# Kernel tuning notes

Measured on AMD Instinct MI355X. Metric: run time of the kernel, lower is better.

## Reference

```python
import jax, jax.numpy as jnp
import numpy as np

N = 4096        # num_queries == gnn_query_dim
C1 = 1001       # classes + 1
D = 4096        # gnn_query_dim
H_MLP = 1024    # mlp_hidden_dim
H = 256         # hidden_dim
O = 256         # output_dim
TOP_K = 32
BN_EPS = 1e-5


def setup_inputs() -> dict:
    key = jax.random.key(0)
    ks = jax.random.split(key, 14)
    def lin(kw, fan_in, shape):
        s = 1.0 / np.sqrt(fan_in)
        return jax.random.uniform(kw, shape, jnp.float32, -s, s)
    return {
        "probs": jax.random.uniform(ks[0], (N, C1), jnp.float32),
        "bbox_coords": jax.random.uniform(ks[1], (N, 4), jnp.float32),
        "query_emb": jax.random.normal(ks[2], (N, D), jnp.float32) * 0.02,
        "node_emb": jax.random.normal(ks[3], (N, D), jnp.float32) * 0.02,
        "mlp_w1": lin(ks[4], D + 4 + C1, (D + 4 + C1, H_MLP)),
        "mlp_b1": lin(ks[5], D + 4 + C1, (H_MLP,)),
        "mlp_w2": lin(ks[6], H_MLP, (H_MLP, N)),
        "mlp_b2": lin(ks[7], H_MLP, (N,)),
        "conv_w1": lin(ks[8], D, (D, H)),
        "conv_b1": lin(ks[9], D, (H,)),
        "conv_w2": lin(ks[10], H, (H, O)),
        "conv_b2": lin(ks[11], H, (O,)),
        "bn_gamma": jnp.ones((H,), jnp.float32),
        "bn_beta": jnp.zeros((H,), jnp.float32),
    }


def reference(probs, bbox_coords, query_emb, node_emb,
              mlp_w1, mlp_b1, mlp_w2, mlp_b2,
              conv_w1, conv_b1, conv_w2, conv_b2,
              bn_gamma, bn_beta):
    # edge-weight MLP -> dense dynamic adjacency logits (N, N)
    ew_in = jnp.concatenate([query_emb, probs, bbox_coords], axis=-1)
    h = jax.nn.relu(ew_in @ mlp_w1 + mlp_b1)
    adj = h @ mlp_w2 + mlp_b2                      # (N, N)

    # top-k neighbors per node (sparse dynamic graph)
    vals, idx = jax.lax.top_k(adj, TOP_K)          # (N, K), (N, K)

    # GCN symmetric normalization from row-degree (sum of top-k weights)
    deg = jnp.sum(vals, axis=-1)                   # (N,)
    dinv = jnp.where(deg > 0, jax.lax.rsqrt(jnp.maximum(deg, 1e-12)), 0.0)
    wn = vals * dinv[:, None] * dinv[idx]          # (N, K)

    def gcn_conv(x, w, b):
        # gather neighbor features, weighted sum, then linear
        msg = jnp.einsum('nk,nkf->nf', wn, x[idx])  # (N, F)
        return msg @ w + b

    out = gcn_conv(node_emb, conv_w1, conv_b1)      # (N, H)
    # BatchNorm1d (batch statistics, training-mode math)
    mean = jnp.mean(out, axis=0)
    var = jnp.var(out, axis=0)
    out = (out - mean) * jax.lax.rsqrt(var + BN_EPS) * bn_gamma + bn_beta
    out = jax.nn.relu(out)
    # dropout is identity in eval mode
    out = gcn_conv(out, conv_w2, conv_b2)           # (N, O)
    return out
```

## Files before the change

kernel.cpp:

```cpp
#include <hip/hip_runtime.h>
#include <cfloat>

#define N_NODES 4096
#define C1_DIM  1001
#define D_DIM   4096
#define HMLP    1024
#define KCAT    (D_DIM + C1_DIM + 4)
#define K1PAD   5120
#define TOPK    32

typedef unsigned short u16;
typedef __bf16 bf16x8 __attribute__((ext_vector_type(8)));
typedef float  f32x4  __attribute__((ext_vector_type(4)));

__device__ __forceinline__ unsigned rne_bits(float x) {
  const unsigned u = __float_as_uint(x);
  return u + 0x7FFFu + ((u >> 16) & 1u);
}

__device__ __forceinline__ void gload16(const void* g, void* l) {
  __builtin_amdgcn_global_load_lds(
      (const __attribute__((address_space(1))) unsigned int*)g,
      (__attribute__((address_space(3))) unsigned int*)l, 16, 0, 0);
}

__device__ __forceinline__ void transpose_body(
    const float* __restrict__ in, int R, int C, int Rpad,
    u16* __restrict__ out_hi, u16* __restrict__ out_lo,
    int bxi, int byi, float (*t)[65]) {
  const int rb = bxi * 64;
  const int cb = byi * 64;
  const int tid = threadIdx.x;
  const int lr = tid >> 6, lc = tid & 63;
#pragma unroll
  for (int i = 0; i < 16; ++i) {
    const int r = lr + i * 4;
    const int gr = rb + r;
    t[r][lc] = (gr < R) ? in[(size_t)gr * C + cb + lc] : 0.f;
  }
  __syncthreads();
#pragma unroll
  for (int i = 0; i < 16; ++i) {
    const int c = lr + i * 4;
    const float v = t[lc][c];
    const unsigned vh = rne_bits(v);
    const float r = v - __uint_as_float(vh & 0xFFFF0000u);
    const size_t o = (size_t)(cb + c) * Rpad + rb + lc;
    out_hi[o] = (u16)(vh >> 16);
    out_lo[o] = (u16)(rne_bits(r) >> 16);
  }
}

__device__ __forceinline__ void a_split_body(
    const float* __restrict__ query, const float* __restrict__ probs,
    const float* __restrict__ bbox,
    u16* __restrict__ hi, u16* __restrict__ lo, int blk) {
  const size_t idx = ((size_t)blk * 256 + threadIdx.x) * 8;
  const int row = (int)(idx / K1PAD);
  const int col = (int)(idx - (size_t)row * K1PAD);
  float xs[8];
  if (col < D_DIM) {
    const float4 x0 = *(const float4*)(query + (size_t)row * D_DIM + col);
    const float4 x1 = *(const float4*)(query + (size_t)row * D_DIM + col + 4);
    xs[0]=x0.x; xs[1]=x0.y; xs[2]=x0.z; xs[3]=x0.w;
    xs[4]=x1.x; xs[5]=x1.y; xs[6]=x1.z; xs[7]=x1.w;
  } else {
#pragma unroll
    for (int e = 0; e < 8; ++e) {
      const int c = col + e - D_DIM;
      xs[e] = (c < C1_DIM) ? probs[(size_t)row * C1_DIM + c]
            : (c < C1_DIM + 4) ? bbox[(size_t)row * 4 + (c - C1_DIM)] : 0.f;
    }
  }
  unsigned hw[4], lw[4];
#pragma unroll
  for (int p = 0; p < 4; ++p) {
    const unsigned v0 = rne_bits(xs[2*p]);
    const unsigned v1 = rne_bits(xs[2*p+1]);
    hw[p] = (v1 & 0xFFFF0000u) | (v0 >> 16);
    const float r0 = xs[2*p]   - __uint_as_float(v0 & 0xFFFF0000u);
    const float r1 = xs[2*p+1] - __uint_as_float(v1 & 0xFFFF0000u);
    lw[p] = (rne_bits(r1) & 0xFFFF0000u) | (rne_bits(r0) >> 16);
  }
  *(uint4*)(hi + idx) = make_uint4(hw[0], hw[1], hw[2], hw[3]);
  *(uint4*)(lo + idx) = make_uint4(lw[0], lw[1], lw[2], lw[3]);
}

__global__ __launch_bounds__(256) void prep1_kernel(
    const float* __restrict__ query, const float* __restrict__ probs,
    const float* __restrict__ bbox, const float* __restrict__ mlp_w1,
    u16* __restrict__ a_hi, u16* __restrict__ a_lo,
    u16* __restrict__ w1t_hi, u16* __restrict__ w1t_lo) {
  __shared__ float t[64][65];
  const int b = blockIdx.x;
  if (b < 10240) {
    a_split_body(query, probs, bbox, a_hi, a_lo, b);
  } else {
    const int bb = b - 10240;
    transpose_body(mlp_w1, KCAT, HMLP, K1PAD, w1t_hi, w1t_lo,
                   bb % 80, bb / 80, t);
  }
}

__global__ __launch_bounds__(256) void prep2_kernel(
    const float* __restrict__ mlp_w2, const float* __restrict__ conv_w1,
    u16* __restrict__ w2t_hi, u16* __restrict__ w2t_lo,
    u16* __restrict__ w1ct_hi, u16* __restrict__ w1ct_lo) {
  __shared__ float t[64][65];
  const int b = blockIdx.x;
  if (b < 1024) {
    transpose_body(mlp_w2, HMLP, N_NODES, HMLP, w2t_hi, w2t_lo,
                   b & 15, b >> 4, t);
  } else {
    const int bb = b - 1024;
    transpose_body(conv_w1, D_DIM, 256, D_DIM, w1ct_hi, w1ct_lo,
                   bb & 63, bb >> 6, t);
  }
}


template<bool RELU, bool OUT_SPLIT, bool HASBIAS>
__device__ __forceinline__ void epilogue_64(
    f32x4 (&acc)[4][2], int row0, int col0, int wr0, int wc0, int lane,
    const float* bias, float* Cf, u16* Chi, u16* Clo, int N) {
#pragma unroll
  for (int mi = 0; mi < 4; ++mi)
#pragma unroll
    for (int ni = 0; ni < 2; ++ni) {
      const int gcol = col0 + wc0 + ni * 16 + (lane & 15);
      const float b = HASBIAS ? bias[gcol] : 0.f;
#pragma unroll
      for (int r = 0; r < 4; ++r) {
        const int grow = row0 + wr0 + mi * 16 + (lane >> 4) * 4 + r;
        float v = acc[mi][ni][r] + b;
        if (RELU) v = fmaxf(v, 0.f);
        if (OUT_SPLIT) {
          const unsigned vh = rne_bits(v);
          Chi[(size_t)grow * N + gcol] = (u16)(vh >> 16);
          const float rr = v - __uint_as_float(vh & 0xFFFF0000u);
          Clo[(size_t)grow * N + gcol] = (u16)(rne_bits(rr) >> 16);
        } else {
          Cf[(size_t)grow * N + gcol] = v;
        }
      }
    }
}

template<bool RELU, bool OUT_SPLIT, bool HASBIAS>
__device__ __forceinline__ void gemm_pipe3(
    int bx, int by,
    const u16* __restrict__ Ahi, const u16* __restrict__ Alo, int lda,
    const u16* __restrict__ Bthi, const u16* __restrict__ Btlo, int ldb,
    const float* __restrict__ bias,
    float* __restrict__ Cf, u16* __restrict__ Chi, u16* __restrict__ Clo,
    int N, int K, u16* lds) {
  const int tid = threadIdx.x;
  const int lane = tid & 63, wave = tid >> 6;
  const int row0 = by * 128, col0 = bx * 64;
  const int wr0 = (wave >> 1) * 64, wc0 = (wave & 1) * 32;
  const int srow = tid >> 2;
  const int sk   = ((tid & 3) ^ ((tid >> 3) & 3)) * 8;
  const int wu   = (tid & ~63) * 8;

  f32x4 acc[4][2];
#pragma unroll
  for (int mi = 0; mi < 4; ++mi)
#pragma unroll
    for (int ni = 0; ni < 2; ++ni) acc[mi][ni] = (f32x4){0.f, 0.f, 0.f, 0.f};

  auto stage = [&](int buf, int k0) {
    u16* base = lds + buf * 12288;
    gload16(Ahi + (size_t)(row0 + srow) * lda + k0 + sk,      base + wu);
    gload16(Ahi + (size_t)(row0 + 64 + srow) * lda + k0 + sk, base + 2048 + wu);
    gload16(Alo + (size_t)(row0 + srow) * lda + k0 + sk,      base + 4096 + wu);
    gload16(Alo + (size_t)(row0 + 64 + srow) * lda + k0 + sk, base + 6144 + wu);
    gload16(Bthi + (size_t)(col0 + srow) * ldb + k0 + sk, base + 8192 + wu);
    gload16(Btlo + (size_t)(col0 + srow) * ldb + k0 + sk, base + 10240 + wu);
  };
  auto compute = [&](int buf) {
    u16* base = lds + buf * 12288;
    const int ko_swz = ((lane >> 4) ^ ((lane >> 1) & 3)) * 8;
    const int ar = lane & 15;
    bf16x8 ah[4], al[4], bh[2], bl[2];
#pragma unroll
    for (int mi = 0; mi < 4; ++mi) {
      const int r = wr0 + mi * 16 + ar;
      ah[mi] = *(const bf16x8*)&base[r * 32 + ko_swz];
      al[mi] = *(const bf16x8*)&base[4096 + r * 32 + ko_swz];
    }
#pragma unroll
    for (int ni = 0; ni < 2; ++ni) {
      const int c = wc0 + ni * 16 + ar;
      bh[ni] = *(const bf16x8*)&base[8192 + c * 32 + ko_swz];
      bl[ni] = *(const bf16x8*)&base[10240 + c * 32 + ko_swz];
    }
#pragma unroll
    for (int mi = 0; mi < 4; ++mi)
#pragma unroll
      for (int ni = 0; ni < 2; ++ni) {
        acc[mi][ni] = __builtin_amdgcn_mfma_f32_16x16x32_bf16(ah[mi], bh[ni], acc[mi][ni], 0, 0, 0);
        acc[mi][ni] = __builtin_amdgcn_mfma_f32_16x16x32_bf16(ah[mi], bl[ni], acc[mi][ni], 0, 0, 0);
        acc[mi][ni] = __builtin_amdgcn_mfma_f32_16x16x32_bf16(al[mi], bh[ni], acc[mi][ni], 0, 0, 0);
      }
  };

  const int nk = K >> 5;
  stage(0, 0);
  stage(1, 32);
  int cb = 0;
  for (int k = 0; k < nk; ++k) {
    if (k + 2 < nk) {
      int sb = cb + 2; if (sb >= 3) sb -= 3;
      stage(sb, (k + 2) * 32);
      asm volatile("s_waitcnt vmcnt(12)" ::: "memory");
    } else if (k + 1 < nk) {
      asm volatile("s_waitcnt vmcnt(6)" ::: "memory");
    } else {
      asm volatile("s_waitcnt vmcnt(0)" ::: "memory");
    }
    __builtin_amdgcn_s_barrier();
    compute(cb);
    __builtin_amdgcn_s_barrier();
    ++cb; if (cb >= 3) cb -= 3;
  }

  epilogue_64<RELU, OUT_SPLIT, HASBIAS>(acc, row0, col0, wr0, wc0, lane,
                                        bias, Cf, Chi, Clo, N);
}

__device__ __forceinline__ void gemm_a1p(
    int bx, int by,
    const float* __restrict__ Aq, int lda,
    const u16* __restrict__ Bthi, const u16* __restrict__ Btlo, int ldb,
    float* __restrict__ Cf, int N, int K, u16* lds) {
  const int tid = threadIdx.x;
  const int lane = tid & 63, wave = tid >> 6;
  const int row0 = by * 128, col0 = bx * 64;
  const int wr0 = (wave >> 1) * 64, wc0 = (wave & 1) * 32;
  const int srow = tid >> 2;
  const int sk   = ((tid & 3) ^ ((tid >> 3) & 3)) * 8;
  const int wu   = (tid & ~63) * 8;
  const int arowA = tid >> 3;
  const int skA   = ((tid & 7) ^ ((tid >> 3) & 7)) * 4;

  f32x4 acc[4][2];
#pragma unroll
  for (int mi = 0; mi < 4; ++mi)
#pragma unroll
    for (int ni = 0; ni < 2; ++ni) acc[mi][ni] = (f32x4){0.f, 0.f, 0.f, 0.f};

  auto stage = [&](int buf, int k0) {
    u16* base = lds + buf * 12288;
#pragma unroll
    for (int j = 0; j < 4; ++j) {
      gload16(Aq + (size_t)(row0 + 32 * j + arowA) * lda + k0 + skA,
              base + j * 2048 + wu);
    }
    gload16(Bthi + (size_t)(col0 + srow) * ldb + k0 + sk, base + 8192 + wu);
    gload16(Btlo + (size_t)(col0 + srow) * ldb + k0 + sk, base + 10240 + wu);
  };
  auto compute = [&](int buf) {
    u16* base = lds + buf * 12288;
    const float* Af = (const float*)base;
    const int ko_swz = ((lane >> 4) ^ ((lane >> 1) & 3)) * 8;
    const int c = lane >> 4;
    const int ar = lane & 15;
    bf16x8 ah[4], al[4], bh[2], bl[2];
#pragma unroll
    for (int mi = 0; mi < 4; ++mi) {
      const int r = wr0 + mi * 16 + ar;
      const int s = ar & 7;
      const f32x4 a0 = *(const f32x4*)&Af[r * 32 + (((2 * c) ^ s) * 4)];
      const f32x4 a1 = *(const f32x4*)&Af[r * 32 + (((2 * c + 1) ^ s) * 4)];
      const float xs[8] = {a0[0], a0[1], a0[2], a0[3], a1[0], a1[1], a1[2], a1[3]};
      union { u16 u[8]; bf16x8 v; } H, L;
#pragma unroll
      for (int e = 0; e < 8; ++e) {
        const unsigned vh = rne_bits(xs[e]);
        H.u[e] = (u16)(vh >> 16);
        const float rr = xs[e] - __uint_as_float(vh & 0xFFFF0000u);
        L.u[e] = (u16)(rne_bits(rr) >> 16);
      }
      ah[mi] = H.v; al[mi] = L.v;
    }
#pragma unroll
    for (int ni = 0; ni < 2; ++ni) {
      const int cc = wc0 + ni * 16 + ar;
      bh[ni] = *(const bf16x8*)&base[8192 + cc * 32 + ko_swz];
      bl[ni] = *(const bf16x8*)&base[10240 + cc * 32 + ko_swz];
    }
#pragma unroll
    for (int mi = 0; mi < 4; ++mi)
#pragma unroll
      for (int ni = 0; ni < 2; ++ni) {
        acc[mi][ni] = __builtin_amdgcn_mfma_f32_16x16x32_bf16(ah[mi], bh[ni], acc[mi][ni], 0, 0, 0);
        acc[mi][ni] = __builtin_amdgcn_mfma_f32_16x16x32_bf16(ah[mi], bl[ni], acc[mi][ni], 0, 0, 0);
        acc[mi][ni] = __builtin_amdgcn_mfma_f32_16x16x32_bf16(al[mi], bh[ni], acc[mi][ni], 0, 0, 0);
      }
  };

  const int nk = K >> 5;
  stage(0, 0);
  stage(1, 32);
  int cb = 0;
  for (int k = 0; k < nk; ++k) {
    if (k + 2 < nk) {
      int sb = cb + 2; if (sb >= 3) sb -= 3;
      stage(sb, (k + 2) * 32);
      asm volatile("s_waitcnt vmcnt(12)" ::: "memory");
    } else if (k + 1 < nk) {
      asm volatile("s_waitcnt vmcnt(6)" ::: "memory");
    } else {
      asm volatile("s_waitcnt vmcnt(0)" ::: "memory");
    }
    __builtin_amdgcn_s_barrier();
    compute(cb);
    __builtin_amdgcn_s_barrier();
    ++cb; if (cb >= 3) cb -= 3;
  }

  epilogue_64<false, false, false>(acc, row0, col0, wr0, wc0, lane,
                                   nullptr, Cf, nullptr, nullptr, N);
}

template<bool HASBIAS>
__device__ __forceinline__ void gemm_pipe128(
    int bx, int by,
    const u16* __restrict__ Ahi, const u16* __restrict__ Alo, int lda,
    const u16* __restrict__ Bthi, const u16* __restrict__ Btlo, int ldb,
    const float* __restrict__ bias, float* __restrict__ Cf,
    int N, int K, u16* lds) {
  const int tid = threadIdx.x;
  const int lane = tid & 63, wave = tid >> 6;
  const int row0 = by * 128, col0 = bx * 128;
  const int wr0 = (wave >> 1) * 64, wc0 = (wave & 1) * 64;
  const int srow = tid >> 2;
  const int sk   = ((tid & 3) ^ ((tid >> 3) & 3)) * 8;
  const int wu   = (tid & ~63) * 8;

  f32x4 acc[4][4];
#pragma unroll
  for (int mi = 0; mi < 4; ++mi)
#pragma unroll
    for (int ni = 0; ni < 4; ++ni) acc[mi][ni] = (f32x4){0.f, 0.f, 0.f, 0.f};

  auto stage = [&](int buf, int k0) {
    u16* base = lds + buf * 16384;
    gload16(Ahi + (size_t)(row0 + srow) * lda + k0 + sk,      base + wu);
    gload16(Ahi + (size_t)(row0 + 64 + srow) * lda + k0 + sk, base + 2048 + wu);
    gload16(Alo + (size_t)(row0 + srow) * lda + k0 + sk,      base + 4096 + wu);
    gload16(Alo + (size_t)(row0 + 64 + srow) * lda + k0 + sk, base + 6144 + wu);
    gload16(Bthi + (size_t)(col0 + srow) * ldb + k0 + sk,      base + 8192 + wu);
    gload16(Bthi + (size_t)(col0 + 64 + srow) * ldb + k0 + sk, base + 10240 + wu);
    gload16(Btlo + (size_t)(col0 + srow) * ldb + k0 + sk,      base + 12288 + wu);
    gload16(Btlo + (size_t)(col0 + 64 + srow) * ldb + k0 + sk, base + 14336 + wu);
  };
  auto compute = [&](int buf) {
    u16* base = lds + buf * 16384;
    const int ko_swz = ((lane >> 4) ^ ((lane >> 1) & 3)) * 8;
    const int ar = lane & 15;
    bf16x8 ah[4], al[4], bh[4], bl[4];
#pragma unroll
    for (int mi = 0; mi < 4; ++mi) {
      const int r = wr0 + mi * 16 + ar;
      ah[mi] = *(const bf16x8*)&base[r * 32 + ko_swz];
      al[mi] = *(const bf16x8*)&base[4096 + r * 32 + ko_swz];
    }
#pragma unroll
    for (int ni = 0; ni < 4; ++ni) {
      const int c = wc0 + ni * 16 + ar;
      bh[ni] = *(const bf16x8*)&base[8192 + c * 32 + ko_swz];
      bl[ni] = *(const bf16x8*)&base[12288 + c * 32 + ko_swz];
    }
#pragma unroll
    for (int mi = 0; mi < 4; ++mi)
#pragma unroll
      for (int ni = 0; ni < 4; ++ni) {
        acc[mi][ni] = __builtin_amdgcn_mfma_f32_16x16x32_bf16(ah[mi], bh[ni], acc[mi][ni], 0, 0, 0);
        acc[mi][ni] = __builtin_amdgcn_mfma_f32_16x16x32_bf16(ah[mi], bl[ni], acc[mi][ni], 0, 0, 0);
        acc[mi][ni] = __builtin_amdgcn_mfma_f32_16x16x32_bf16(al[mi], bh[ni], acc[mi][ni], 0, 0, 0);
      }
  };

  const int nk = K >> 5;
  stage(0, 0);
  int cur = 0;
  for (int k = 0; k < nk; ++k) {
    if (k + 1 < nk) {
      stage(cur ^ 1, (k + 1) * 32);
      asm volatile("s_waitcnt vmcnt(8)" ::: "memory");
    } else {
      asm volatile("s_waitcnt vmcnt(0)" ::: "memory");
    }
    __builtin_amdgcn_s_barrier();
    compute(cur);
    __builtin_amdgcn_s_barrier();
    cur ^= 1;
  }

#pragma unroll
  for (int mi = 0; mi < 4; ++mi)
#pragma unroll
    for (int ni = 0; ni < 4; ++ni) {
      const int gcol = col0 + wc0 + ni * 16 + (lane & 15);
      const float b = HASBIAS ? bias[gcol] : 0.f;
#pragma unroll
      for (int r = 0; r < 4; ++r) {
        const int grow = row0 + wr0 + mi * 16 + (lane >> 4) * 4 + r;
        Cf[(size_t)grow * N + gcol] = acc[mi][ni][r] + b;
      }
    }
}

__global__ __launch_bounds__(256, 2) void gemm1_kernel(
    const u16* __restrict__ a_hi, const u16* __restrict__ a_lo,
    const u16* __restrict__ w1t_hi, const u16* __restrict__ w1t_lo,
    const float* __restrict__ b1,
    u16* __restrict__ h_hi, u16* __restrict__ h_lo) {
  __shared__ u16 lds[3 * 12288];
  const int r = blockIdx.x;
  const int x = r & 7;
  const int i = r >> 3;
  const int by = x * 4 + (i >> 4);
  const int bx = i & 15;
  gemm_pipe3<true, true, true>(bx, by,
      a_hi, a_lo, K1PAD, w1t_hi, w1t_lo, K1PAD, b1,
      nullptr, h_hi, h_lo, HMLP, K1PAD, lds);
}

__global__ __launch_bounds__(256, 2) void fused2_kernel(
    const u16* __restrict__ h_hi, const u16* __restrict__ h_lo,
    const u16* __restrict__ w2t_hi, const u16* __restrict__ w2t_lo,
    const float* __restrict__ b2, float* __restrict__ adj,
    const float* __restrict__ node,
    const u16* __restrict__ w1ct_hi, const u16* __restrict__ w1ct_lo,
    float* __restrict__ Z1) {
  __shared__ u16 lds[3 * 12288];
  const int bid = blockIdx.x;
  if (bid < 128) {
    const int x = bid & 7;
    const int i = bid >> 3;
    const int by = x * 4 + (i >> 2);
    const int bx = i & 3;
    gemm_a1p(bx, by,
             node, D_DIM, w1ct_hi, w1ct_lo, D_DIM,
             Z1, 256, D_DIM, lds);
  } else {
    const int r = bid - 128;
    const int x = r & 7;
    const int i = r >> 3;
    const int rg = x >> 1, cg = x & 1;
    const int by = rg * 8 + (i >> 4);
    const int bx = cg * 16 + (i & 15);
    gemm_pipe128<true>(bx, by,
        h_hi, h_lo, HMLP, w2t_hi, w2t_lo, HMLP, b2,
        adj, N_NODES, HMLP, lds);
  }
}

__global__ __launch_bounds__(256) void gemm_small_bn(
    const float* __restrict__ A, const float* __restrict__ colstats,
    const float* __restrict__ gamma, const float* __restrict__ beta,
    const float* __restrict__ B, float* __restrict__ C,
    int M, int Ncols, int K) {
  __shared__ float As[16][68];
  __shared__ float Bs[16][68];
  const int tid = threadIdx.x;
  const int row0 = blockIdx.y * 64, col0 = blockIdx.x * 64;
  const int tx = tid & 15, ty = tid >> 4;
  const int arow = tid >> 2, acol = (tid & 3) * 4;
  const int brow = tid >> 4, bcol = (tid & 15) * 4;

  float acc[4][4];
#pragma unroll
  for (int i = 0; i < 4; ++i)
#pragma unroll
    for (int j = 0; j < 4; ++j) acc[i][j] = 0.f;

  for (int k0 = 0; k0 < K; k0 += 16) {
    float4 a4 = *(const float4*)(A + (size_t)(row0 + arow) * K + k0 + acol);
    float av4[4] = {a4.x, a4.y, a4.z, a4.w};
#pragma unroll
    for (int e = 0; e < 4; ++e) {
      const int c = k0 + acol + e;
      const float mean = colstats[c] * (1.f / 4096.f);
      float var = colstats[256 + c] * (1.f / 4096.f) - mean * mean;
      var = fmaxf(var, 0.f);
      const float v = (av4[e] - mean) * rsqrtf(var + 1e-5f) * gamma[c] + beta[c];
      av4[e] = fmaxf(v, 0.f);
    }
    const float4 b4 = *(const float4*)(B + (size_t)(k0 + brow) * Ncols + col0 + bcol);
    __syncthreads();
    As[acol + 0][arow] = av4[0]; As[acol + 1][arow] = av4[1];
    As[acol + 2][arow] = av4[2]; As[acol + 3][arow] = av4[3];
    *(float4*)&Bs[brow][bcol] = b4;
    __syncthreads();
#pragma unroll
    for (int k = 0; k < 16; ++k) {
      float av[4], bw[4];
      *(float4*)&av[0] = *(const float4*)&As[k][ty * 4];
      *(float4*)&bw[0] = *(const float4*)&Bs[k][tx * 4];
#pragma unroll
      for (int i = 0; i < 4; ++i)
#pragma unroll
        for (int j = 0; j < 4; ++j) acc[i][j] += av[i] * bw[j];
    }
  }

#pragma unroll
  for (int i = 0; i < 4; ++i) {
    const int r = row0 + ty * 4 + i;
    float4 v;
    v.x = acc[i][0]; v.y = acc[i][1]; v.z = acc[i][2]; v.w = acc[i][3];
    *(float4*)(C + (size_t)r * Ncols + col0 + tx * 4) = v;
  }
}

__global__ __launch_bounds__(256) void topk_kernel(
    const float* __restrict__ adj, float* __restrict__ vals,
    int* __restrict__ idxo, float* __restrict__ dinv) {
  __shared__ float sv[N_NODES];
  __shared__ float rw[4];
  __shared__ int   iw[4];
  const int n = blockIdx.x, tid = threadIdx.x;
  const int lane = tid & 63, wave = tid >> 6;
  const float4* rowp = (const float4*)(adj + (size_t)n * N_NODES);

  float mv = -FLT_MAX; int mi = 0x7FFFFFFF;
  for (int g = tid; g < N_NODES / 4; g += 256) {
    const float4 v4 = rowp[g];
    *(float4*)&sv[g * 4] = v4;
    if (v4.x > mv) { mv = v4.x; mi = g * 4 + 0; }
    if (v4.y > mv) { mv = v4.y; mi = g * 4 + 1; }
    if (v4.z > mv) { mv = v4.z; mi = g * 4 + 2; }
    if (v4.w > mv) { mv = v4.w; mi = g * 4 + 3; }
  }

  float sum = 0.f;
  for (int it = 0; it < TOPK; ++it) {
    float bv = mv; int bi = mi;
#pragma unroll
    for (int off = 1; off < 64; off <<= 1) {
      const float ov = __shfl_xor(bv, off);
      const int   oi = __shfl_xor(bi, off);
      if (ov > bv || (ov == bv && oi < bi)) { bv = ov; bi = oi; }
    }
    if (lane == 0) { rw[wave] = bv; iw[wave] = bi; }
    __syncthreads();
    bv = rw[0]; bi = iw[0];
#pragma unroll
    for (int w = 1; w < 4; ++w) {
      const float ov = rw[w]; const int oi = iw[w];
      if (ov > bv || (ov == bv && oi < bi)) { bv = ov; bi = oi; }
    }
    if (tid == 0) {
      vals[(size_t)n * TOPK + it] = bv;
      idxo[(size_t)n * TOPK + it] = bi;
    }
    sum += bv;
    if (tid == ((bi >> 2) & 255)) {
      sv[bi] = -FLT_MAX;
      mv = -FLT_MAX; mi = 0x7FFFFFFF;
      for (int g = tid; g < N_NODES / 4; g += 256) {
#pragma unroll
        for (int e = 0; e < 4; ++e) {
          const float v = sv[g * 4 + e];
          if (v > mv) { mv = v; mi = g * 4 + e; }
        }
      }
    }
    __syncthreads();
  }
  if (tid == 0)
    dinv[n] = (sum > 0.f) ? rsqrtf(fmaxf(sum, 1e-12f)) : 0.f;
}

__global__ __launch_bounds__(256) void agg_kernel(
    const float* __restrict__ Z, const float* __restrict__ vals,
    const int* __restrict__ idxo, const float* __restrict__ dinv,
    const float* __restrict__ bias, float* __restrict__ out) {
  const int n = blockIdx.x, f = threadIdx.x;
  const float dn = dinv[n];
  float acc = bias[f];
#pragma unroll
  for (int k = 0; k < TOPK; ++k) {
    const int   j = idxo[n * TOPK + k];
    const float w = vals[n * TOPK + k] * dn * dinv[j];
    acc += w * Z[(size_t)j * 256 + f];
  }
  out[(size_t)n * 256 + f] = acc;
}

__global__ __launch_bounds__(256) void bn_partial(
    const float* __restrict__ x, float* __restrict__ partial) {
  const int b = blockIdx.x, c = threadIdx.x;
  float s = 0.f, s2 = 0.f;
  for (int r = b * 32; r < b * 32 + 32; ++r) {
    const float v = x[(size_t)r * 256 + c];
    s += v; s2 += v * v;
  }
  partial[(size_t)b * 512 + c]       = s;
  partial[(size_t)b * 512 + 256 + c] = s2;
}

__global__ __launch_bounds__(256) void bn_reduce(
    const float* __restrict__ partial, float* __restrict__ colstats) {
  const int j = blockIdx.x, t = threadIdx.x;
  __shared__ float red[128];
  if (t < 128) red[t] = partial[(size_t)t * 512 + j];
  __syncthreads();
  for (int s = 64; s > 0; s >>= 1) {
    if (t < s) red[t] += red[t + s];
    __syncthreads();
  }
  if (t == 0) colstats[j] = red[0];
}

extern "C" void kernel_launch(void* const* d_in, const int* in_sizes, int n_in,
                              void* d_out, int out_size, void* d_ws, size_t ws_size,
                              hipStream_t stream) {
  const float* probs   = (const float*)d_in[0];
  const float* bbox    = (const float*)d_in[1];
  const float* query   = (const float*)d_in[2];
  const float* node    = (const float*)d_in[3];
  const float* mlp_w1  = (const float*)d_in[4];
  const float* mlp_b1  = (const float*)d_in[5];
  const float* mlp_w2  = (const float*)d_in[6];
  const float* mlp_b2  = (const float*)d_in[7];
  const float* conv_w1 = (const float*)d_in[8];
  const float* conv_b1 = (const float*)d_in[9];
  const float* conv_w2 = (const float*)d_in[10];
  const float* conv_b2 = (const float*)d_in[11];
  const float* gamma   = (const float*)d_in[12];
  const float* beta    = (const float*)d_in[13];

  float* ws = (float*)d_ws;
  size_t off = 0;
  float* R1 = ws + off;  off += (size_t)N_NODES * K1PAD;
  u16* a_hi = (u16*)R1;
  u16* a_lo = a_hi + (size_t)N_NODES * K1PAD;
  float* adj = R1;
  float* spare = R1 + (size_t)N_NODES * N_NODES;
  float* Z1   = spare;
  float* vals = spare + (size_t)N_NODES * 256;
  int*   idxo = (int*)(vals + (size_t)N_NODES * TOPK);
  float* dinv = (float*)idxo + (size_t)N_NODES * TOPK;
  float* partial  = dinv + N_NODES;
  float* colstats = partial + 128 * 512;
  float* R2 = ws + off;  off += (size_t)HMLP * K1PAD;
  u16* w1t_hi = (u16*)R2;
  u16* w1t_lo = w1t_hi + (size_t)HMLP * K1PAD;
  u16* w2t_hi = (u16*)R2;
  u16* w2t_lo = w2t_hi + (size_t)N_NODES * HMLP;
  u16* w1ct_hi = (u16*)(R2 + (size_t)N_NODES * HMLP);
  u16* w1ct_lo = w1ct_hi + (size_t)256 * D_DIM;
  float* out1 = R2 + (size_t)N_NODES * HMLP;
  float* R3 = ws + off;  off += (size_t)N_NODES * HMLP;
  u16* h_hi = (u16*)R3;
  u16* h_lo = h_hi + (size_t)N_NODES * HMLP;
  float* Z2 = adj;

  prep1_kernel<<<10240 + 1280, 256, 0, stream>>>(
      query, probs, bbox, mlp_w1, a_hi, a_lo, w1t_hi, w1t_lo);
  gemm1_kernel<<<512, 256, 0, stream>>>(
      a_hi, a_lo, w1t_hi, w1t_lo, mlp_b1, h_hi, h_lo);
  prep2_kernel<<<1024 + 256, 256, 0, stream>>>(
      mlp_w2, conv_w1, w2t_hi, w2t_lo, w1ct_hi, w1ct_lo);
  fused2_kernel<<<128 + (N_NODES / 128) * (N_NODES / 128), 256, 0, stream>>>(
      h_hi, h_lo, w2t_hi, w2t_lo, mlp_b2, adj, node, w1ct_hi, w1ct_lo, Z1);
  topk_kernel<<<N_NODES, 256, 0, stream>>>(adj, vals, idxo, dinv);
  agg_kernel<<<N_NODES, 256, 0, stream>>>(Z1, vals, idxo, dinv, conv_b1, out1);
  bn_partial<<<128, 256, 0, stream>>>(out1, partial);
  bn_reduce<<<512, 256, 0, stream>>>(partial, colstats);
  gemm_small_bn<<<dim3(256 / 64, N_NODES / 64), 256, 0, stream>>>(
      out1, colstats, gamma, beta, conv_w2, Z2, N_NODES, 256, 256);
  agg_kernel<<<N_NODES, 256, 0, stream>>>(Z2, vals, idxo, dinv, conv_b2, (float*)d_out);
}
```

Measured before the change: 521.6 us.

## Enlarge adjacency GEMM tile to 256x256 with 512-thread blocks

```diff
diff --git a/kernel.cpp b/kernel.cpp
--- a/kernel.cpp
+++ b/kernel.cpp
@@ -229,11 +229,11 @@
 }
 
 __device__ __forceinline__ void gemm_a1p(
-    int bx, int by,
+    int ltid, int bx, int by,
     const float* __restrict__ Aq, int lda,
     const u16* __restrict__ Bthi, const u16* __restrict__ Btlo, int ldb,
     float* __restrict__ Cf, int N, int K, u16* lds) {
-  const int tid = threadIdx.x;
+  const int tid = ltid;
   const int lane = tid & 63, wave = tid >> 6;
   const int row0 = by * 128, col0 = bx * 64;
   const int wr0 = (wave >> 1) * 64, wc0 = (wave & 1) * 32;
@@ -321,95 +321,6 @@
 
   epilogue_64<false, false, false>(acc, row0, col0, wr0, wc0, lane,
                                    nullptr, Cf, nullptr, nullptr, N);
-}
-
-template<bool HASBIAS>
-__device__ __forceinline__ void gemm_pipe128(
-    int bx, int by,
-    const u16* __restrict__ Ahi, const u16* __restrict__ Alo, int lda,
-    const u16* __restrict__ Bthi, const u16* __restrict__ Btlo, int ldb,
-    const float* __restrict__ bias, float* __restrict__ Cf,
-    int N, int K, u16* lds) {
-  const int tid = threadIdx.x;
-  const int lane = tid & 63, wave = tid >> 6;
-  const int row0 = by * 128, col0 = bx * 128;
-  const int wr0 = (wave >> 1) * 64, wc0 = (wave & 1) * 64;
-  const int srow = tid >> 2;
-  const int sk   = ((tid & 3) ^ ((tid >> 3) & 3)) * 8;
-  const int wu   = (tid & ~63) * 8;
-
-  f32x4 acc[4][4];
-#pragma unroll
-  for (int mi = 0; mi < 4; ++mi)
-#pragma unroll
-    for (int ni = 0; ni < 4; ++ni) acc[mi][ni] = (f32x4){0.f, 0.f, 0.f, 0.f};
-
-  auto stage = [&](int buf, int k0) {
-    u16* base = lds + buf * 16384;
-    gload16(Ahi + (size_t)(row0 + srow) * lda + k0 + sk,      base + wu);
-    gload16(Ahi + (size_t)(row0 + 64 + srow) * lda + k0 + sk, base + 2048 + wu);
-    gload16(Alo + (size_t)(row0 + srow) * lda + k0 + sk,      base + 4096 + wu);
-    gload16(Alo + (size_t)(row0 + 64 + srow) * lda + k0 + sk, base + 6144 + wu);
-    gload16(Bthi + (size_t)(col0 + srow) * ldb + k0 + sk,      base + 8192 + wu);
-    gload16(Bthi + (size_t)(col0 + 64 + srow) * ldb + k0 + sk, base + 10240 + wu);
-    gload16(Btlo + (size_t)(col0 + srow) * ldb + k0 + sk,      base + 12288 + wu);
-    gload16(Btlo + (size_t)(col0 + 64 + srow) * ldb + k0 + sk, base + 14336 + wu);
-  };
-  auto compute = [&](int buf) {
-    u16* base = lds + buf * 16384;
-    const int ko_swz = ((lane >> 4) ^ ((lane >> 1) & 3)) * 8;
-    const int ar = lane & 15;
-    bf16x8 ah[4], al[4], bh[4], bl[4];
-#pragma unroll
-    for (int mi = 0; mi < 4; ++mi) {
-      const int r = wr0 + mi * 16 + ar;
-      ah[mi] = *(const bf16x8*)&base[r * 32 + ko_swz];
-      al[mi] = *(const bf16x8*)&base[4096 + r * 32 + ko_swz];
-    }
-#pragma unroll
-    for (int ni = 0; ni < 4; ++ni) {
-      const int c = wc0 + ni * 16 + ar;
-      bh[ni] = *(const bf16x8*)&base[8192 + c * 32 + ko_swz];
-      bl[ni] = *(const bf16x8*)&base[12288 + c * 32 + ko_swz];
-    }
-#pragma unroll
-    for (int mi = 0; mi < 4; ++mi)
-#pragma unroll
-      for (int ni = 0; ni < 4; ++ni) {
-        acc[mi][ni] = __builtin_amdgcn_mfma_f32_16x16x32_bf16(ah[mi], bh[ni], acc[mi][ni], 0, 0, 0);
-        acc[mi][ni] = __builtin_amdgcn_mfma_f32_16x16x32_bf16(ah[mi], bl[ni], acc[mi][ni], 0, 0, 0);
-        acc[mi][ni] = __builtin_amdgcn_mfma_f32_16x16x32_bf16(al[mi], bh[ni], acc[mi][ni], 0, 0, 0);
-      }
-  };
-
-  const int nk = K >> 5;
-  stage(0, 0);
-  int cur = 0;
-  for (int k = 0; k < nk; ++k) {
-    if (k + 1 < nk) {
-      stage(cur ^ 1, (k + 1) * 32);
-      asm volatile("s_waitcnt vmcnt(8)" ::: "memory");
-    } else {
-      asm volatile("s_waitcnt vmcnt(0)" ::: "memory");
-    }
-    __builtin_amdgcn_s_barrier();
-    compute(cur);
-    __builtin_amdgcn_s_barrier();
-    cur ^= 1;
-  }
-
-#pragma unroll
-  for (int mi = 0; mi < 4; ++mi)
-#pragma unroll
-    for (int ni = 0; ni < 4; ++ni) {
-      const int gcol = col0 + wc0 + ni * 16 + (lane & 15);
-      const float b = HASBIAS ? bias[gcol] : 0.f;
-#pragma unroll
-      for (int r = 0; r < 4; ++r) {
-        const int grow = row0 + wr0 + mi * 16 + (lane >> 4) * 4 + r;
-        Cf[(size_t)grow * N + gcol] = acc[mi][ni][r] + b;
-      }
-    }
 }
 
 __global__ __launch_bounds__(256, 2) void gemm1_kernel(
@@ -428,34 +339,112 @@
       nullptr, h_hi, h_lo, HMLP, K1PAD, lds);
 }
 
-__global__ __launch_bounds__(256, 2) void fused2_kernel(
+__global__ __launch_bounds__(512, 1) void adj_kernel(
     const u16* __restrict__ h_hi, const u16* __restrict__ h_lo,
     const u16* __restrict__ w2t_hi, const u16* __restrict__ w2t_lo,
     const float* __restrict__ b2, float* __restrict__ adj,
     const float* __restrict__ node,
     const u16* __restrict__ w1ct_hi, const u16* __restrict__ w1ct_lo,
     float* __restrict__ Z1) {
-  __shared__ u16 lds[3 * 12288];
+  __shared__ u16 lds[73728];
   const int bid = blockIdx.x;
-  if (bid < 128) {
-    const int x = bid & 7;
-    const int i = bid >> 3;
-    const int by = x * 4 + (i >> 2);
-    const int bx = i & 3;
-    gemm_a1p(bx, by,
+  if (bid < 64) {
+    const int half = threadIdx.x >> 8;
+    const int ltid = threadIdx.x & 255;
+    const int by = bid >> 1;
+    const int bx = (bid & 1) * 2 + half;
+    gemm_a1p(ltid, bx, by,
              node, D_DIM, w1ct_hi, w1ct_lo, D_DIM,
-             Z1, 256, D_DIM, lds);
-  } else {
-    const int r = bid - 128;
-    const int x = r & 7;
-    const int i = r >> 3;
-    const int rg = x >> 1, cg = x & 1;
-    const int by = rg * 8 + (i >> 4);
-    const int bx = cg * 16 + (i & 15);
-    gemm_pipe128<true>(bx, by,
-        h_hi, h_lo, HMLP, w2t_hi, w2t_lo, HMLP, b2,
-        adj, N_NODES, HMLP, lds);
-  }
+             Z1, 256, D_DIM, lds + half * 36864);
+    return;
+  }
+  const int r = bid - 64;
+  const int x = r & 7;
+  const int i = r >> 3;
+  const int rg = x >> 1, cg = x & 1;
+  const int by = rg * 4 + (i >> 3);
+  const int bx = cg * 8 + (i & 7);
+
+  const int lda = HMLP, ldb = HMLP, N = N_NODES, K = HMLP;
+  const int tid = threadIdx.x;
+  const int lane = tid & 63, wave = tid >> 6;
+  const int row0 = by * 256, col0 = bx * 256;
+  const int wr0 = (wave >> 2) * 128;
+  const int wc0 = (wave & 3) * 64;
+  const int srow = tid >> 2;
+  const int sk   = ((tid & 3) ^ ((tid >> 3) & 3)) * 8;
+  const int wu   = (tid & ~63) * 8;
+
+  f32x4 acc[8][4];
+#pragma unroll
+  for (int mi = 0; mi < 8; ++mi)
+#pragma unroll
+    for (int ni = 0; ni < 4; ++ni) acc[mi][ni] = (f32x4){0.f, 0.f, 0.f, 0.f};
+
+  auto stage = [&](int buf, int k0) {
+    u16* base = lds + buf * 32768;
+    gload16(h_hi + (size_t)(row0 + srow) * lda + k0 + sk,       base + wu);
+    gload16(h_hi + (size_t)(row0 + 128 + srow) * lda + k0 + sk, base + 4096 + wu);
+    gload16(h_lo + (size_t)(row0 + srow) * lda + k0 + sk,       base + 8192 + wu);
+    gload16(h_lo + (size_t)(row0 + 128 + srow) * lda + k0 + sk, base + 12288 + wu);
+    gload16(w2t_hi + (size_t)(col0 + srow) * ldb + k0 + sk,       base + 16384 + wu);
+    gload16(w2t_hi + (size_t)(col0 + 128 + srow) * ldb + k0 + sk, base + 20480 + wu);
+    gload16(w2t_lo + (size_t)(col0 + srow) * ldb + k0 + sk,       base + 24576 + wu);
+    gload16(w2t_lo + (size_t)(col0 + 128 + srow) * ldb + k0 + sk, base + 28672 + wu);
+  };
+  auto compute = [&](int buf) {
+    u16* base = lds + buf * 32768;
+    const int ko_swz = ((lane >> 4) ^ ((lane >> 1) & 3)) * 8;
+    const int ar = lane & 15;
+    bf16x8 bh[4], bl[4];
+#pragma unroll
+    for (int ni = 0; ni < 4; ++ni) {
+      const int c = wc0 + ni * 16 + ar;
+      bh[ni] = *(const bf16x8*)&base[16384 + c * 32 + ko_swz];
+      bl[ni] = *(const bf16x8*)&base[24576 + c * 32 + ko_swz];
+    }
+#pragma unroll
+    for (int mi = 0; mi < 8; ++mi) {
+      const int rr2 = wr0 + mi * 16 + ar;
+      const bf16x8 ah = *(const bf16x8*)&base[rr2 * 32 + ko_swz];
+      const bf16x8 al = *(const bf16x8*)&base[8192 + rr2 * 32 + ko_swz];
+#pragma unroll
+      for (int ni = 0; ni < 4; ++ni) {
+        acc[mi][ni] = __builtin_amdgcn_mfma_f32_16x16x32_bf16(ah, bh[ni], acc[mi][ni], 0, 0, 0);
+        acc[mi][ni] = __builtin_amdgcn_mfma_f32_16x16x32_bf16(ah, bl[ni], acc[mi][ni], 0, 0, 0);
+        acc[mi][ni] = __builtin_amdgcn_mfma_f32_16x16x32_bf16(al, bh[ni], acc[mi][ni], 0, 0, 0);
+      }
+    }
+  };
+
+  const int nk = K >> 5;
+  stage(0, 0);
+  int cur = 0;
+  for (int k = 0; k < nk; ++k) {
+    if (k + 1 < nk) {
+      stage(cur ^ 1, (k + 1) * 32);
+      asm volatile("s_waitcnt vmcnt(8)" ::: "memory");
+    } else {
+      asm volatile("s_waitcnt vmcnt(0)" ::: "memory");
+    }
+    __builtin_amdgcn_s_barrier();
+    compute(cur);
+    __builtin_amdgcn_s_barrier();
+    cur ^= 1;
+  }
+
+#pragma unroll
+  for (int mi = 0; mi < 8; ++mi)
+#pragma unroll
+    for (int ni = 0; ni < 4; ++ni) {
+      const int gcol = col0 + wc0 + ni * 16 + (lane & 15);
+      const float b = b2[gcol];
+#pragma unroll
+      for (int rr3 = 0; rr3 < 4; ++rr3) {
+        const int grow = row0 + wr0 + mi * 16 + (lane >> 4) * 4 + rr3;
+        adj[(size_t)grow * N + gcol] = acc[mi][ni][rr3] + b;
+      }
+    }
 }
 
 __global__ __launch_bounds__(256) void gemm_small_bn(
@@ -666,7 +655,7 @@
       a_hi, a_lo, w1t_hi, w1t_lo, mlp_b1, h_hi, h_lo);
   prep2_kernel<<<1024 + 256, 256, 0, stream>>>(
       mlp_w2, conv_w1, w2t_hi, w2t_lo, w1ct_hi, w1ct_lo);
-  fused2_kernel<<<128 + (N_NODES / 128) * (N_NODES / 128), 256, 0, stream>>>(
+  adj_kernel<<<320, 512, 0, stream>>>(
       h_hi, h_lo, w2t_hi, w2t_lo, mlp_b2, adj, node, w1ct_hi, w1ct_lo, Z1);
   topk_kernel<<<N_NODES, 256, 0, stream>>>(adj, vals, idxo, dinv);
   agg_kernel<<<N_NODES, 256, 0, stream>>>(Z1, vals, idxo, dinv, conv_b1, out1);
```

Result: slower. 601.9 us (+15.4%).

## Fuse fp32 activation hi/lo split into first MLP GEMM instead of prep pass

Applied to the files above, without the earlier changes.

```diff
diff --git a/kernel.cpp b/kernel.cpp
--- a/kernel.cpp
+++ b/kernel.cpp
@@ -51,52 +51,35 @@
   }
 }
 
-__device__ __forceinline__ void a_split_body(
-    const float* __restrict__ query, const float* __restrict__ probs,
-    const float* __restrict__ bbox,
-    u16* __restrict__ hi, u16* __restrict__ lo, int blk) {
-  const size_t idx = ((size_t)blk * 256 + threadIdx.x) * 8;
-  const int row = (int)(idx / K1PAD);
-  const int col = (int)(idx - (size_t)row * K1PAD);
-  float xs[8];
-  if (col < D_DIM) {
-    const float4 x0 = *(const float4*)(query + (size_t)row * D_DIM + col);
-    const float4 x1 = *(const float4*)(query + (size_t)row * D_DIM + col + 4);
-    xs[0]=x0.x; xs[1]=x0.y; xs[2]=x0.z; xs[3]=x0.w;
-    xs[4]=x1.x; xs[5]=x1.y; xs[6]=x1.z; xs[7]=x1.w;
-  } else {
-#pragma unroll
-    for (int e = 0; e < 8; ++e) {
-      const int c = col + e - D_DIM;
-      xs[e] = (c < C1_DIM) ? probs[(size_t)row * C1_DIM + c]
-            : (c < C1_DIM + 4) ? bbox[(size_t)row * 4 + (c - C1_DIM)] : 0.f;
-    }
-  }
-  unsigned hw[4], lw[4];
-#pragma unroll
-  for (int p = 0; p < 4; ++p) {
-    const unsigned v0 = rne_bits(xs[2*p]);
-    const unsigned v1 = rne_bits(xs[2*p+1]);
-    hw[p] = (v1 & 0xFFFF0000u) | (v0 >> 16);
-    const float r0 = xs[2*p]   - __uint_as_float(v0 & 0xFFFF0000u);
-    const float r1 = xs[2*p+1] - __uint_as_float(v1 & 0xFFFF0000u);
-    lw[p] = (rne_bits(r1) & 0xFFFF0000u) | (rne_bits(r0) >> 16);
-  }
-  *(uint4*)(hi + idx) = make_uint4(hw[0], hw[1], hw[2], hw[3]);
-  *(uint4*)(lo + idx) = make_uint4(lw[0], lw[1], lw[2], lw[3]);
+__device__ __forceinline__ void tailf_body(
+    const float* __restrict__ probs, const float* __restrict__ bbox,
+    float* __restrict__ tailF, int blk) {
+  const int i = blk * 256 + threadIdx.x;
+  const int row = i >> 7;
+  const int col = (i & 127) * 8;
+  float v[8];
+#pragma unroll
+  for (int e = 0; e < 8; ++e) {
+    const int c = col + e;
+    v[e] = (c < C1_DIM) ? probs[(size_t)row * C1_DIM + c]
+         : (c < C1_DIM + 4) ? bbox[(size_t)row * 4 + (c - C1_DIM)] : 0.f;
+  }
+  float* dst = tailF + (size_t)row * 1024 + col;
+  *(float4*)dst       = make_float4(v[0], v[1], v[2], v[3]);
+  *(float4*)(dst + 4) = make_float4(v[4], v[5], v[6], v[7]);
 }
 
 __global__ __launch_bounds__(256) void prep1_kernel(
-    const float* __restrict__ query, const float* __restrict__ probs,
-    const float* __restrict__ bbox, const float* __restrict__ mlp_w1,
-    u16* __restrict__ a_hi, u16* __restrict__ a_lo,
+    const float* __restrict__ probs, const float* __restrict__ bbox,
+    const float* __restrict__ mlp_w1,
+    float* __restrict__ tailF,
     u16* __restrict__ w1t_hi, u16* __restrict__ w1t_lo) {
   __shared__ float t[64][65];
   const int b = blockIdx.x;
-  if (b < 10240) {
-    a_split_body(query, probs, bbox, a_hi, a_lo, b);
+  if (b < 2048) {
+    tailf_body(probs, bbox, tailF, b);
   } else {
-    const int bb = b - 10240;
+    const int bb = b - 2048;
     transpose_body(mlp_w1, KCAT, HMLP, K1PAD, w1t_hi, w1t_lo,
                    bb % 80, bb / 80, t);
   }
@@ -146,10 +129,10 @@
     }
 }
 
-template<bool RELU, bool OUT_SPLIT, bool HASBIAS>
-__device__ __forceinline__ void gemm_pipe3(
+template<bool RELU, bool OUT_SPLIT, bool HASBIAS, bool SPLITSRC>
+__device__ __forceinline__ void gemm_a1p(
     int bx, int by,
-    const u16* __restrict__ Ahi, const u16* __restrict__ Alo, int lda,
+    const float* __restrict__ Aq, int lda, const float* __restrict__ Atail,
     const u16* __restrict__ Bthi, const u16* __restrict__ Btlo, int ldb,
     const float* __restrict__ bias,
     float* __restrict__ Cf, u16* __restrict__ Chi, u16* __restrict__ Clo,
@@ -161,6 +144,8 @@
   const int srow = tid >> 2;
   const int sk   = ((tid & 3) ^ ((tid >> 3) & 3)) * 8;
   const int wu   = (tid & ~63) * 8;
+  const int arowA = tid >> 3;
+  const int skA   = ((tid & 7) ^ ((tid >> 3) & 7)) * 4;
 
   f32x4 acc[4][2];
 #pragma unroll
@@ -170,29 +155,46 @@
 
   auto stage = [&](int buf, int k0) {
     u16* base = lds + buf * 12288;
-    gload16(Ahi + (size_t)(row0 + srow) * lda + k0 + sk,      base + wu);
-    gload16(Ahi + (size_t)(row0 + 64 + srow) * lda + k0 + sk, base + 2048 + wu);
-    gload16(Alo + (size_t)(row0 + srow) * lda + k0 + sk,      base + 4096 + wu);
-    gload16(Alo + (size_t)(row0 + 64 + srow) * lda + k0 + sk, base + 6144 + wu);
+    const float* srcA = Aq;
+    int ldaA = lda, kk = k0;
+    if (SPLITSRC && k0 >= D_DIM) { srcA = Atail; ldaA = 1024; kk = k0 - D_DIM; }
+#pragma unroll
+    for (int j = 0; j < 4; ++j) {
+      gload16(srcA + (size_t)(row0 + 32 * j + arowA) * ldaA + kk + skA,
+              base + j * 2048 + wu);
+    }
     gload16(Bthi + (size_t)(col0 + srow) * ldb + k0 + sk, base + 8192 + wu);
     gload16(Btlo + (size_t)(col0 + srow) * ldb + k0 + sk, base + 10240 + wu);
   };
   auto compute = [&](int buf) {
     u16* base = lds + buf * 12288;
+    const float* Af = (const float*)base;
     const int ko_swz = ((lane >> 4) ^ ((lane >> 1) & 3)) * 8;
+    const int c = lane >> 4;
     const int ar = lane & 15;
     bf16x8 ah[4], al[4], bh[2], bl[2];
 #pragma unroll
     for (int mi = 0; mi < 4; ++mi) {
       const int r = wr0 + mi * 16 + ar;
-      ah[mi] = *(const bf16x8*)&base[r * 32 + ko_swz];
-      al[mi] = *(const bf16x8*)&base[4096 + r * 32 + ko_swz];
+      const int s = ar & 7;
+      const f32x4 a0 = *(const f32x4*)&Af[r * 32 + (((2 * c) ^ s) * 4)];
+      const f32x4 a1 = *(const f32x4*)&Af[r * 32 + (((2 * c + 1) ^ s) * 4)];
+      const float xs[8] = {a0[0], a0[1], a0[2], a0[3], a1[0], a1[1], a1[2], a1[3]};
+      union { u16 u[8]; bf16x8 v; } H, L;
+#pragma unroll
+      for (int e = 0; e < 8; ++e) {
+        const unsigned vh = rne_bits(xs[e]);
+        H.u[e] = (u16)(vh >> 16);
+        const float rr = xs[e] - __uint_as_float(vh & 0xFFFF0000u);
+        L.u[e] = (u16)(rne_bits(rr) >> 16);
+      }
+      ah[mi] = H.v; al[mi] = L.v;
     }
 #pragma unroll
     for (int ni = 0; ni < 2; ++ni) {
-      const int c = wc0 + ni * 16 + ar;
-      bh[ni] = *(const bf16x8*)&base[8192 + c * 32 + ko_swz];
-      bl[ni] = *(const bf16x8*)&base[10240 + c * 32 + ko_swz];
+      const int cc = wc0 + ni * 16 + ar;
+      bh[ni] = *(const bf16x8*)&base[8192 + cc * 32 + ko_swz];
+      bl[ni] = *(const bf16x8*)&base[10240 + cc * 32 + ko_swz];
     }
 #pragma unroll
     for (int mi = 0; mi < 4; ++mi)
@@ -226,101 +228,6 @@
 
   epilogue_64<RELU, OUT_SPLIT, HASBIAS>(acc, row0, col0, wr0, wc0, lane,
                                         bias, Cf, Chi, Clo, N);
-}
-
-__device__ __forceinline__ void gemm_a1p(
-    int bx, int by,
-    const float* __restrict__ Aq, int lda,
-    const u16* __restrict__ Bthi, const u16* __restrict__ Btlo, int ldb,
-    float* __restrict__ Cf, int N, int K, u16* lds) {
-  const int tid = threadIdx.x;
-  const int lane = tid & 63, wave = tid >> 6;
-  const int row0 = by * 128, col0 = bx * 64;
-  const int wr0 = (wave >> 1) * 64, wc0 = (wave & 1) * 32;
-  const int srow = tid >> 2;
-  const int sk   = ((tid & 3) ^ ((tid >> 3) & 3)) * 8;
-  const int wu   = (tid & ~63) * 8;
-  const int arowA = tid >> 3;
-  const int skA   = ((tid & 7) ^ ((tid >> 3) & 7)) * 4;
-
-  f32x4 acc[4][2];
-#pragma unroll
-  for (int mi = 0; mi < 4; ++mi)
-#pragma unroll
-    for (int ni = 0; ni < 2; ++ni) acc[mi][ni] = (f32x4){0.f, 0.f, 0.f, 0.f};
-
-  auto stage = [&](int buf, int k0) {
-    u16* base = lds + buf * 12288;
-#pragma unroll
-    for (int j = 0; j < 4; ++j) {
-      gload16(Aq + (size_t)(row0 + 32 * j + arowA) * lda + k0 + skA,
-              base + j * 2048 + wu);
-    }
-    gload16(Bthi + (size_t)(col0 + srow) * ldb + k0 + sk, base + 8192 + wu);
-    gload16(Btlo + (size_t)(col0 + srow) * ldb + k0 + sk, base + 10240 + wu);
-  };
-  auto compute = [&](int buf) {
-    u16* base = lds + buf * 12288;
-    const float* Af = (const float*)base;
-    const int ko_swz = ((lane >> 4) ^ ((lane >> 1) & 3)) * 8;
-    const int c = lane >> 4;
-    const int ar = lane & 15;
-    bf16x8 ah[4], al[4], bh[2], bl[2];
-#pragma unroll
-    for (int mi = 0; mi < 4; ++mi) {
-      const int r = wr0 + mi * 16 + ar;
-      const int s = ar & 7;
-      const f32x4 a0 = *(const f32x4*)&Af[r * 32 + (((2 * c) ^ s) * 4)];
-      const f32x4 a1 = *(const f32x4*)&Af[r * 32 + (((2 * c + 1) ^ s) * 4)];
-      const float xs[8] = {a0[0], a0[1], a0[2], a0[3], a1[0], a1[1], a1[2], a1[3]};
-      union { u16 u[8]; bf16x8 v; } H, L;
-#pragma unroll
-      for (int e = 0; e < 8; ++e) {
-        const unsigned vh = rne_bits(xs[e]);
-        H.u[e] = (u16)(vh >> 16);
-        const float rr = xs[e] - __uint_as_float(vh & 0xFFFF0000u);
-        L.u[e] = (u16)(rne_bits(rr) >> 16);
-      }
-      ah[mi] = H.v; al[mi] = L.v;
-    }
-#pragma unroll
-    for (int ni = 0; ni < 2; ++ni) {
-      const int cc = wc0 + ni * 16 + ar;
-      bh[ni] = *(const bf16x8*)&base[8192 + cc * 32 + ko_swz];
-      bl[ni] = *(const bf16x8*)&base[10240 + cc * 32 + ko_swz];
-    }
-#pragma unroll
-    for (int mi = 0; mi < 4; ++mi)
-#pragma unroll
-      for (int ni = 0; ni < 2; ++ni) {
-        acc[mi][ni] = __builtin_amdgcn_mfma_f32_16x16x32_bf16(ah[mi], bh[ni], acc[mi][ni], 0, 0, 0);
-        acc[mi][ni] = __builtin_amdgcn_mfma_f32_16x16x32_bf16(ah[mi], bl[ni], acc[mi][ni], 0, 0, 0);
-        acc[mi][ni] = __builtin_amdgcn_mfma_f32_16x16x32_bf16(al[mi], bh[ni], acc[mi][ni], 0, 0, 0);
-      }
-  };
-
-  const int nk = K >> 5;
-  stage(0, 0);
-  stage(1, 32);
-  int cb = 0;
-  for (int k = 0; k < nk; ++k) {
-    if (k + 2 < nk) {
-      int sb = cb + 2; if (sb >= 3) sb -= 3;
-      stage(sb, (k + 2) * 32);
-      asm volatile("s_waitcnt vmcnt(12)" ::: "memory");
-    } else if (k + 1 < nk) {
-      asm volatile("s_waitcnt vmcnt(6)" ::: "memory");
-    } else {
-      asm volatile("s_waitcnt vmcnt(0)" ::: "memory");
-    }
-    __builtin_amdgcn_s_barrier();
-    compute(cb);
-    __builtin_amdgcn_s_barrier();
-    ++cb; if (cb >= 3) cb -= 3;
-  }
-
-  epilogue_64<false, false, false>(acc, row0, col0, wr0, wc0, lane,
-                                   nullptr, Cf, nullptr, nullptr, N);
 }
 
 template<bool HASBIAS>
@@ -413,7 +320,7 @@
 }
 
 __global__ __launch_bounds__(256, 2) void gemm1_kernel(
-    const u16* __restrict__ a_hi, const u16* __restrict__ a_lo,
+    const float* __restrict__ query, const float* __restrict__ tailF,
     const u16* __restrict__ w1t_hi, const u16* __restrict__ w1t_lo,
     const float* __restrict__ b1,
     u16* __restrict__ h_hi, u16* __restrict__ h_lo) {
@@ -423,8 +330,8 @@
   const int i = r >> 3;
   const int by = x * 4 + (i >> 4);
   const int bx = i & 15;
-  gemm_pipe3<true, true, true>(bx, by,
-      a_hi, a_lo, K1PAD, w1t_hi, w1t_lo, K1PAD, b1,
+  gemm_a1p<true, true, true, true>(bx, by,
+      query, D_DIM, tailF, w1t_hi, w1t_lo, K1PAD, b1,
       nullptr, h_hi, h_lo, HMLP, K1PAD, lds);
 }
 
@@ -442,9 +349,9 @@
     const int i = bid >> 3;
     const int by = x * 4 + (i >> 2);
     const int bx = i & 3;
-    gemm_a1p(bx, by,
-             node, D_DIM, w1ct_hi, w1ct_lo, D_DIM,
-             Z1, 256, D_DIM, lds);
+    gemm_a1p<false, false, false, false>(bx, by,
+        node, D_DIM, nullptr, w1ct_hi, w1ct_lo, D_DIM, nullptr,
+        Z1, nullptr, nullptr, 256, D_DIM, lds);
   } else {
     const int r = bid - 128;
     const int x = r & 7;
@@ -637,8 +544,7 @@
   float* ws = (float*)d_ws;
   size_t off = 0;
   float* R1 = ws + off;  off += (size_t)N_NODES * K1PAD;
-  u16* a_hi = (u16*)R1;
-  u16* a_lo = a_hi + (size_t)N_NODES * K1PAD;
+  float* tailF = R1;
   float* adj = R1;
   float* spare = R1 + (size_t)N_NODES * N_NODES;
   float* Z1   = spare;
@@ -660,10 +566,10 @@
   u16* h_lo = h_hi + (size_t)N_NODES * HMLP;
   float* Z2 = adj;
 
-  prep1_kernel<<<10240 + 1280, 256, 0, stream>>>(
-      query, probs, bbox, mlp_w1, a_hi, a_lo, w1t_hi, w1t_lo);
+  prep1_kernel<<<2048 + 1280, 256, 0, stream>>>(
+      probs, bbox, mlp_w1, tailF, w1t_hi, w1t_lo);
   gemm1_kernel<<<512, 256, 0, stream>>>(
-      a_hi, a_lo, w1t_hi, w1t_lo, mlp_b1, h_hi, h_lo);
+      query, tailF, w1t_hi, w1t_lo, mlp_b1, h_hi, h_lo);
   prep2_kernel<<<1024 + 256, 256, 0, stream>>>(
       mlp_w2, conv_w1, w2t_hi, w2t_lo, w1ct_hi, w1ct_lo);
   fused2_kernel<<<128 + (N_NODES / 128) * (N_NODES / 128), 256, 0, stream>>>(
```

Result: slower. 591.1 us (+13.3%).
